# Performance work log

Hardware: AMD Instinct MI355X
Metric: run time of the kernel (lower is better)

Reference implementation:

```python
import jax, jax.numpy as jnp
import numpy as np

D_MODEL = 512
D_AUX = 64
B, N = 8, 2048


def setup_inputs() -> dict:
    key = jax.random.key(0)
    ks = jax.random.split(key, 12)
    lim = 1.0 / np.sqrt(D_MODEL)  # torch Linear default init scale
    inp = {
        "x": jax.random.normal(ks[0], (B, N, D_MODEL), dtype=jnp.float32),
        "query_aux": jax.random.normal(ks[1], (B, N, D_AUX), dtype=jnp.float32),
        "key_aux": jax.random.normal(ks[2], (B, N, D_AUX), dtype=jnp.float32),
        "adjacency_mask": jax.random.randint(ks[3], (B, N, N), 0, 2, dtype=jnp.int32),
        "merge_coefficients": jnp.float32(0.3),
        "Wq": jax.random.uniform(ks[4], (D_MODEL, D_MODEL), jnp.float32, -lim, lim),
        "bq": jax.random.uniform(ks[5], (D_MODEL,), jnp.float32, -lim, lim),
        "Wk": jax.random.uniform(ks[6], (D_MODEL, D_MODEL), jnp.float32, -lim, lim),
        "bk": jax.random.uniform(ks[7], (D_MODEL,), jnp.float32, -lim, lim),
        "Wv": jax.random.uniform(ks[8], (D_MODEL, D_MODEL), jnp.float32, -lim, lim),
        "bv": jax.random.uniform(ks[9], (D_MODEL,), jnp.float32, -lim, lim),
        "threshold": jnp.float32(0.5),
    }
    return inp


def reference(x, query_aux, key_aux, adjacency_mask, merge_coefficients,
              Wq, bq, Wk, bk, Wv, bv, threshold):
    d_model = x.shape[-1]
    d_aux = key_aux.shape[-1]
    scale = jnp.asarray(d_model, x.dtype) ** 0.5
    scale_aux = jnp.asarray(d_aux, x.dtype) ** 0.5

    q = x @ Wq.T + bq  # [B,N,D]
    k = x @ Wk.T + bk
    v = x @ Wv.T + bv

    scores = jnp.einsum('bnd,bmd->bnm', q, k) / scale  # [B,N,N]
    scores_aux = jnp.einsum('bnd,bmd->bnm', query_aux, key_aux) / scale_aux

    # data-dependent merge: where aux score nonzero AND score above learned threshold
    merge_mask = (scores_aux != 0) & (scores > threshold)
    merged = (1.0 - merge_coefficients) * scores + merge_coefficients * scores_aux
    scores = jnp.where(merge_mask, merged, scores)

    mask_value = jnp.finfo(scores.dtype).min
    scores = jnp.where(adjacency_mask == 0, mask_value, scores)

    weights = jax.nn.softmax(scores, axis=-1)
    return jnp.einsum('bnm,bmd->bnd', weights, v)
```

## Files before the change

kernel.cpp:

```cpp
#include <hip/hip_runtime.h>
#include <cstdint>

#define SEQ    2048
#define DM     512
#define DAUX   64

typedef _Float16 f16;
typedef __attribute__((ext_vector_type(2))) _Float16 f16x2;
typedef __attribute__((ext_vector_type(4))) _Float16 f16x4;
typedef __attribute__((ext_vector_type(8))) _Float16 f16x8;
typedef __attribute__((ext_vector_type(4))) float fx4;
typedef __attribute__((ext_vector_type(16))) float fx16;

__device__ __forceinline__ void g2l16(const void* g, void* l) {
  __builtin_amdgcn_global_load_lds(
      (__attribute__((address_space(1))) void*)const_cast<void*>(g),
      (__attribute__((address_space(3))) void*)l, 16, 0, 0);
}

__device__ __forceinline__ void stagec(const f16* __restrict__ hi,
                                       const f16* __restrict__ lo,
                                       int stride, f16* lds, int t) {
#pragma unroll
  for (int p = 0; p < 4; ++p) {
    int L = p * 256 + t;
    int row = L >> 3, jb = L & 7;
    int jl = jb ^ (row & 7);
    const f16* src = (jl < 4) ? hi + (size_t)row * stride + jl * 8
                              : lo + (size_t)row * stride + (jl - 4) * 8;
    g2l16(src, lds + L * 8);
  }
}
__device__ __forceinline__ f16x8 fragc(const f16* lds, int row, int jl) {
  int jp = jl ^ (row & 7);
  return *(const f16x8*)(lds + row * 64 + jp * 8);
}

__device__ __forceinline__ void stage64(const f16* __restrict__ g0, int stride,
                                        f16* lds, int t) {
#pragma unroll
  for (int p = 0; p < 4; ++p) {
    int L = p * 256 + t;
    int row = L >> 3, jb = L & 7;
    int jl = jb ^ (row & 7);
    g2l16(g0 + (size_t)row * stride + jl * 8, lds + L * 8);
  }
}
__device__ __forceinline__ f16x8 frag64(const f16* lds, int row, int kq) {
  int jp = (kq >> 3) ^ (row & 7);
  return *(const f16x8*)(lds + row * 64 + jp * 8);
}

__device__ __forceinline__ void chunk3c(const f16* A, const f16* B,
                                        fx16 acc[2][2], int wm, int wn, int lane) {
  const int r31 = lane & 31;
  const int half8 = (lane >> 5) * 8;
#pragma unroll
  for (int k0 = 0; k0 < 32; k0 += 16) {
    int kb = (k0 + half8) >> 3;
    f16x8 ah[2], al[2];
#pragma unroll
    for (int it = 0; it < 2; ++it) {
      int row = wm * 64 + it * 32 + r31;
      ah[it] = fragc(A, row, kb);
      al[it] = fragc(A, row, kb + 4);
    }
#pragma unroll
    for (int jt = 0; jt < 2; ++jt) {
      int col = wn * 64 + jt * 32 + r31;
      f16x8 bh = fragc(B, col, kb);
      f16x8 bl = fragc(B, col, kb + 4);
#pragma unroll
      for (int it = 0; it < 2; ++it) {
        acc[it][jt] = __builtin_amdgcn_mfma_f32_32x32x16_f16(ah[it], bh, acc[it][jt], 0, 0, 0);
        acc[it][jt] = __builtin_amdgcn_mfma_f32_32x32x16_f16(ah[it], bl, acc[it][jt], 0, 0, 0);
        acc[it][jt] = __builtin_amdgcn_mfma_f32_32x32x16_f16(al[it], bh, acc[it][jt], 0, 0, 0);
      }
    }
  }
}

__device__ __forceinline__ void chunk1_64(const f16* A, const f16* B,
                                          fx16 acc[2][2], int wm, int wn, int lane) {
  const int r31 = lane & 31;
  const int kq = (lane >> 5) * 8;
#pragma unroll
  for (int k0 = 0; k0 < 64; k0 += 16) {
    f16x8 a[2];
#pragma unroll
    for (int it = 0; it < 2; ++it)
      a[it] = frag64(A, wm * 64 + it * 32 + r31, k0 + kq);
#pragma unroll
    for (int jt = 0; jt < 2; ++jt) {
      f16x8 b = frag64(B, wn * 64 + jt * 32 + r31, k0 + kq);
#pragma unroll
      for (int it = 0; it < 2; ++it)
        acc[it][jt] = __builtin_amdgcn_mfma_f32_32x32x16_f16(a[it], b, acc[it][jt], 0, 0, 0);
    }
  }
}

__global__ __launch_bounds__(256) void convert_split(
    const float* __restrict__ x, const float* __restrict__ Wq,
    const float* __restrict__ Wk, const float* __restrict__ Wv,
    f16* __restrict__ xh, f16* __restrict__ xl,
    f16* __restrict__ Wh, f16* __restrict__ Wl) {
  int idx = blockIdx.x * 256 + threadIdx.x;
  const float* src; f16* dh; f16* dl; size_t off;
  if (idx < 2097152) { src = x; off = (size_t)idx; dh = xh; dl = xl; }
  else {
    int rr = idx - 2097152;
    int w = rr >> 16, o = rr & 65535;
    src = (w == 0) ? Wq : (w == 1) ? Wk : Wv;
    off = (size_t)o;
    dh = Wh + (size_t)w * 262144; dl = Wl + (size_t)w * 262144;
  }
  float4 v = ((const float4*)src)[off];
  float vv[4] = {v.x, v.y, v.z, v.w};
  f16x4 hv, lv;
#pragma unroll
  for (int i = 0; i < 4; ++i) {
    float s = vv[i] * 32.0f;
    f16 hi = (f16)s;
    hv[i] = hi;
    lv[i] = (f16)(s - (float)hi);
  }
  *(f16x4*)(dh + off * 4) = hv;
  *(f16x4*)(dl + off * 4) = lv;
}

__global__ __launch_bounds__(256, 3) void qkv_mfma(
    const f16* __restrict__ xh, const f16* __restrict__ xl,
    const f16* __restrict__ Wh, const f16* __restrict__ Wl,
    const float* __restrict__ bq, const float* __restrict__ bk, const float* __restrict__ bv,
    f16* __restrict__ qh, f16* __restrict__ ql,
    f16* __restrict__ kh, f16* __restrict__ kl,
    f16* __restrict__ vt) {
  __shared__ __align__(16) f16 sm[16384];
  const int t = threadIdx.x;
  const int i0 = blockIdx.x * 128, j0 = blockIdx.y * 128, z = blockIdx.z;
  const f16* WhZ = Wh + (size_t)z * 262144;
  const f16* WlZ = Wl + (size_t)z * 262144;
  const int lane = t & 63, wave = t >> 6;
  const int wm = wave >> 1, wn = wave & 1;
  const int r31 = lane & 31, half = lane >> 5;
  fx16 acc[2][2] = {};
  const f16* xhB = xh + (size_t)i0 * DM;
  const f16* xlB = xl + (size_t)i0 * DM;
  const f16* WhB = WhZ + (size_t)j0 * DM;
  const f16* WlB = WlZ + (size_t)j0 * DM;
  if (z < 2) {
    for (int c = 0; c < 16; ++c) {
      int d0 = c * 32;
      __syncthreads();
      stagec(xhB + d0, xlB + d0, DM, sm, t);
      stagec(WhB + d0, WlB + d0, DM, sm + 8192, t);
      __syncthreads();
      chunk3c(sm, sm + 8192, acc, wm, wn, lane);
    }
  } else {
    for (int c = 0; c < 8; ++c) {
      int d0 = c * 64;
      __syncthreads();
      stage64(xhB + d0, DM, sm, t);
      stage64(WhB + d0, DM, sm + 8192, t);
      __syncthreads();
      chunk1_64(sm, sm + 8192, acc, wm, wn, lane);
    }
  }
  const float* bias = (z == 0) ? bq : (z == 1) ? bk : bv;
  if (z < 2) {
    f16* oh = z ? kh : qh;  f16* ol = z ? kl : ql;
#pragma unroll
    for (int it = 0; it < 2; ++it)
#pragma unroll
      for (int jt = 0; jt < 2; ++jt) {
        int j = j0 + wn * 64 + jt * 32 + r31;
        float bj = bias[j];
#pragma unroll
        for (int r = 0; r < 16; ++r) {
          int ib = i0 + wm * 64 + it * 32 + (r & 3) + 8 * (r >> 2) + 4 * half;
          float val = acc[it][jt][r] * (1.0f / 1024.0f) + bj;
          float s = val * 32.0f;
          f16 hi = (f16)s;
          oh[(size_t)ib * DM + j] = hi;
          ol[(size_t)ib * DM + j] = (f16)(s - (float)hi);
        }
      }
  } else {
#pragma unroll
    for (int it = 0; it < 2; ++it)
#pragma unroll
      for (int jt = 0; jt < 2; ++jt) {
        int j = j0 + wn * 64 + jt * 32 + r31;
        float bj = bias[j];
#pragma unroll
        for (int q4 = 0; q4 < 4; ++q4) {
          int ib = i0 + wm * 64 + it * 32 + 8 * q4 + 4 * half;
          int bb = ib >> 11, nb = ib & 2047;
          f16x4 hv;
#pragma unroll
          for (int g = 0; g < 4; ++g)
            hv[g] = (f16)(acc[it][jt][q4 * 4 + g] * (1.0f / 1024.0f) + bj);
          *(f16x4*)(vt + ((size_t)(bb * DM + j)) * SEQ + nb) = hv;
        }
      }
  }
}

__global__ __launch_bounds__(256, 3) void scores_mfma(
    const f16* __restrict__ qh, const f16* __restrict__ ql,
    const f16* __restrict__ kh, const f16* __restrict__ kl,
    const float* __restrict__ qa, const float* __restrict__ ka,
    const int* __restrict__ adj,
    const float* __restrict__ mc_p, const float* __restrict__ thr_p,
    f16* __restrict__ S16) {
  __shared__ __align__(16) f16 sm[16384];
  const int t = threadIdx.x;
  const int n0 = blockIdx.x * 128, m0 = blockIdx.y * 128, b = blockIdx.z;
  const int lane = t & 63, wave = t >> 6;
  const int wm = wave >> 1, wn = wave & 1;
  const int r31 = lane & 31, half = lane >> 5;
  const int kq = half * 8;

  const f16* qhB = qh + ((size_t)b * SEQ + n0) * DM;
  const f16* qlB = ql + ((size_t)b * SEQ + n0) * DM;
  const f16* khB = kh + ((size_t)b * SEQ + m0) * DM;
  const f16* klB = kl + ((size_t)b * SEQ + m0) * DM;

  fx16 acc[2][2] = {};
  for (int c = 0; c < 16; ++c) {
    int d0 = c * 32;
    __syncthreads();
    stagec(qhB + d0, qlB + d0, DM, sm, t);
    stagec(khB + d0, klB + d0, DM, sm + 8192, t);
    __syncthreads();
    chunk3c(sm, sm + 8192, acc, wm, wn, lane);
  }

  __syncthreads();
  f16* QAl = sm;
  f16* KAl = sm + 8192;
  const float* QAb = qa + ((size_t)b * SEQ + n0) * DAUX;
  const float* KAb = ka + ((size_t)b * SEQ + m0) * DAUX;
#pragma unroll
  for (int p = 0; p < 4; ++p) {
    int L8 = p * 256 + t;
    int row = L8 >> 3, jb = L8 & 7;
    int c8 = jb * 8;
    int jp = jb ^ (row & 7);
    float4 u0 = *(const float4*)(QAb + (size_t)row * DAUX + c8);
    float4 u1 = *(const float4*)(QAb + (size_t)row * DAUX + c8 + 4);
    f16x8 hq = {(f16)u0.x,(f16)u0.y,(f16)u0.z,(f16)u0.w,(f16)u1.x,(f16)u1.y,(f16)u1.z,(f16)u1.w};
    *(f16x8*)(QAl + row * 64 + jp * 8) = hq;
    float4 w0 = *(const float4*)(KAb + (size_t)row * DAUX + c8);
    float4 w1 = *(const float4*)(KAb + (size_t)row * DAUX + c8 + 4);
    f16x8 hk = {(f16)w0.x,(f16)w0.y,(f16)w0.z,(f16)w0.w,(f16)w1.x,(f16)w1.y,(f16)w1.z,(f16)w1.w};
    *(f16x8*)(KAl + row * 64 + jp * 8) = hk;
  }
  __syncthreads();
  fx16 aacc[2][2] = {};
#pragma unroll
  for (int k0 = 0; k0 < 64; k0 += 16) {
    f16x8 qaf[2];
#pragma unroll
    for (int it = 0; it < 2; ++it)
      qaf[it] = frag64(QAl, wm * 64 + it * 32 + r31, k0 + kq);
#pragma unroll
    for (int jt = 0; jt < 2; ++jt) {
      f16x8 kaf = frag64(KAl, wn * 64 + jt * 32 + r31, k0 + kq);
#pragma unroll
      for (int it = 0; it < 2; ++it)
        aacc[it][jt] = __builtin_amdgcn_mfma_f32_32x32x16_f16(qaf[it], kaf, aacc[it][jt], 0, 0, 0);
    }
  }

  const float mc = *mc_p, thr = *thr_p;
  const float invC = 1.0f / (1024.0f * 22.62741699796952f);
#pragma unroll
  for (int it = 0; it < 2; ++it)
#pragma unroll
    for (int jt = 0; jt < 2; ++jt) {
      int col = m0 + wn * 64 + jt * 32 + r31;
#pragma unroll
      for (int r = 0; r < 16; ++r) {
        int row = n0 + wm * 64 + it * 32 + (r & 3) + 8 * (r >> 2) + 4 * half;
        size_t rbase = ((size_t)b * SEQ + row) * SEQ;
        float s = acc[it][jt][r] * invC;
        float sa = aacc[it][jt][r] * 0.125f;
        if (sa != 0.0f && s > thr) s = (1.0f - mc) * s + mc * sa;
        if (adj[rbase + col] == 0) s = -65504.0f;
        S16[rbase + col] = (f16)s;
      }
    }
}

__global__ __launch_bounds__(256) void softmax_p(
    f16* __restrict__ S16, float* __restrict__ rowsum) {
  const int wv = threadIdx.x >> 6, ln = threadIdx.x & 63;
  const size_t row = (size_t)blockIdx.x * 4 + wv;
  f16* Sr = S16 + row * SEQ;
  f16x8 v[4];
  float vals[32];
#pragma unroll
  for (int j = 0; j < 4; ++j) {
    v[j] = *(const f16x8*)(Sr + j * 512 + ln * 8);
#pragma unroll
    for (int i = 0; i < 8; ++i) vals[j * 8 + i] = (float)v[j][i];
  }
  float m = vals[0];
#pragma unroll
  for (int i = 1; i < 32; ++i) m = fmaxf(m, vals[i]);
#pragma unroll
  for (int off = 1; off < 64; off <<= 1) m = fmaxf(m, __shfl_xor(m, off, 64));
  float z = 0.f;
  f16x8 p16[4];
#pragma unroll
  for (int j = 0; j < 4; ++j)
#pragma unroll
    for (int i = 0; i < 8; ++i) {
      f16 p = (f16)(__expf(vals[j * 8 + i] - m) * 1024.0f);
      p16[j][i] = p;
      z += (float)p;
    }
#pragma unroll
  for (int off = 1; off < 64; off <<= 1) z += __shfl_xor(z, off, 64);
  if (ln == 0) rowsum[row] = z;
#pragma unroll
  for (int j = 0; j < 4; ++j)
    *(f16x8*)(Sr + j * 512 + ln * 8) = p16[j];
}

__global__ __launch_bounds__(256, 3) void pv_mfma(
    const f16* __restrict__ P16, const f16* __restrict__ vt,
    const float* __restrict__ rowsum, float* __restrict__ O) {
  __shared__ __align__(16) f16 sm[16384];
  const int t = threadIdx.x;
  const int n0 = blockIdx.x * 128, d0 = blockIdx.y * 128, b = blockIdx.z;
  const int lane = t & 63, wave = t >> 6;
  const int wm = wave >> 1, wn = wave & 1;
  const int r31 = lane & 31, half = lane >> 5;
  fx16 acc[2][2] = {};
  const f16* Pb = P16 + ((size_t)b * SEQ + n0) * SEQ;
  const f16* Vb = vt + ((size_t)b * DM + d0) * SEQ;
  for (int c = 0; c < 32; ++c) {
    int m0 = c * 64;
    __syncthreads();
    stage64(Pb + m0, SEQ, sm, t);
    stage64(Vb + m0, SEQ, sm + 8192, t);
    __syncthreads();
    chunk1_64(sm, sm + 8192, acc, wm, wn, lane);
  }
#pragma unroll
  for (int it = 0; it < 2; ++it)
#pragma unroll
    for (int jt = 0; jt < 2; ++jt) {
      int d = d0 + wn * 64 + jt * 32 + r31;
#pragma unroll
      for (int r = 0; r < 16; ++r) {
        int n = n0 + wm * 64 + it * 32 + (r & 3) + 8 * (r >> 2) + 4 * half;
        float inv = 1.0f / rowsum[(size_t)b * SEQ + n];
        O[((size_t)b * SEQ + n) * DM + d] = acc[it][jt][r] * inv;
      }
    }
}

extern "C" void kernel_launch(void* const* d_in, const int* in_sizes, int n_in,
                              void* d_out, int out_size, void* d_ws, size_t ws_size,
                              hipStream_t stream) {
  const float* x   = (const float*)d_in[0];
  const float* qa  = (const float*)d_in[1];
  const float* ka  = (const float*)d_in[2];
  const int*   adj = (const int*)d_in[3];
  const float* mc  = (const float*)d_in[4];
  const float* Wq  = (const float*)d_in[5];
  const float* bq  = (const float*)d_in[6];
  const float* Wk  = (const float*)d_in[7];
  const float* bk  = (const float*)d_in[8];
  const float* Wv  = (const float*)d_in[9];
  const float* bv  = (const float*)d_in[10];
  const float* thr = (const float*)d_in[11];
  float* out = (float*)d_out;

  f16* qh  = (f16*)d_ws;
  f16* ql  = qh + 8388608;
  f16* kh  = ql + 8388608;
  f16* kl  = kh + 8388608;
  f16* vt  = kl + 8388608;
  f16* S16 = vt + 8388608;
  float* rowsum = (float*)(S16 + 33554432);
  f16* xh = S16;
  f16* xl = xh + 8388608;
  f16* Wh = xl + 8388608;
  f16* Wl = Wh + 786432;

  convert_split<<<8960, 256, 0, stream>>>(x, Wq, Wk, Wv, xh, xl, Wh, Wl);
  qkv_mfma<<<dim3(128, 4, 3), 256, 0, stream>>>(xh, xl, Wh, Wl, bq, bk, bv,
                                                qh, ql, kh, kl, vt);
  scores_mfma<<<dim3(16, 16, 8), 256, 0, stream>>>(qh, ql, kh, kl, qa, ka, adj,
                                                   mc, thr, S16);
  softmax_p<<<4096, 256, 0, stream>>>(S16, rowsum);
  pv_mfma<<<dim3(16, 4, 8), 256, 0, stream>>>(S16, vt, rowsum, out);
}
```

Before: 557.1 us.

## Replace LDS-staged GEMM tiles with register double-buffered direct global loads

```diff
diff --git a/kernel.cpp b/kernel.cpp
--- a/kernel.cpp
+++ b/kernel.cpp
@@ -9,94 +9,69 @@
 typedef __attribute__((ext_vector_type(2))) _Float16 f16x2;
 typedef __attribute__((ext_vector_type(4))) _Float16 f16x4;
 typedef __attribute__((ext_vector_type(8))) _Float16 f16x8;
-typedef __attribute__((ext_vector_type(4))) float fx4;
 typedef __attribute__((ext_vector_type(16))) float fx16;
 
-__device__ __forceinline__ void g2l16(const void* g, void* l) {
-  __builtin_amdgcn_global_load_lds(
-      (__attribute__((address_space(1))) void*)const_cast<void*>(g),
-      (__attribute__((address_space(3))) void*)l, 16, 0, 0);
-}
-
-__device__ __forceinline__ void stagec(const f16* __restrict__ hi,
-                                       const f16* __restrict__ lo,
-                                       int stride, f16* lds, int t) {
-#pragma unroll
-  for (int p = 0; p < 4; ++p) {
-    int L = p * 256 + t;
-    int row = L >> 3, jb = L & 7;
-    int jl = jb ^ (row & 7);
-    const f16* src = (jl < 4) ? hi + (size_t)row * stride + jl * 8
-                              : lo + (size_t)row * stride + (jl - 4) * 8;
-    g2l16(src, lds + L * 8);
-  }
-}
-__device__ __forceinline__ f16x8 fragc(const f16* lds, int row, int jl) {
-  int jp = jl ^ (row & 7);
-  return *(const f16x8*)(lds + row * 64 + jp * 8);
-}
-
-__device__ __forceinline__ void stage64(const f16* __restrict__ g0, int stride,
-                                        f16* lds, int t) {
-#pragma unroll
-  for (int p = 0; p < 4; ++p) {
-    int L = p * 256 + t;
-    int row = L >> 3, jb = L & 7;
-    int jl = jb ^ (row & 7);
-    g2l16(g0 + (size_t)row * stride + jl * 8, lds + L * 8);
-  }
-}
-__device__ __forceinline__ f16x8 frag64(const f16* lds, int row, int kq) {
-  int jp = (kq >> 3) ^ (row & 7);
-  return *(const f16x8*)(lds + row * 64 + jp * 8);
-}
-
-__device__ __forceinline__ void chunk3c(const f16* A, const f16* B,
-                                        fx16 acc[2][2], int wm, int wn, int lane) {
-  const int r31 = lane & 31;
-  const int half8 = (lane >> 5) * 8;
-#pragma unroll
-  for (int k0 = 0; k0 < 32; k0 += 16) {
-    int kb = (k0 + half8) >> 3;
-    f16x8 ah[2], al[2];
-#pragma unroll
-    for (int it = 0; it < 2; ++it) {
-      int row = wm * 64 + it * 32 + r31;
-      ah[it] = fragc(A, row, kb);
-      al[it] = fragc(A, row, kb + 4);
-    }
-#pragma unroll
-    for (int jt = 0; jt < 2; ++jt) {
-      int col = wn * 64 + jt * 32 + r31;
-      f16x8 bh = fragc(B, col, kb);
-      f16x8 bl = fragc(B, col, kb + 4);
-#pragma unroll
-      for (int it = 0; it < 2; ++it) {
-        acc[it][jt] = __builtin_amdgcn_mfma_f32_32x32x16_f16(ah[it], bh, acc[it][jt], 0, 0, 0);
-        acc[it][jt] = __builtin_amdgcn_mfma_f32_32x32x16_f16(ah[it], bl, acc[it][jt], 0, 0, 0);
-        acc[it][jt] = __builtin_amdgcn_mfma_f32_32x32x16_f16(al[it], bh, acc[it][jt], 0, 0, 0);
-      }
-    }
-  }
-}
-
-__device__ __forceinline__ void chunk1_64(const f16* A, const f16* B,
-                                          fx16 acc[2][2], int wm, int wn, int lane) {
-  const int r31 = lane & 31;
-  const int kq = (lane >> 5) * 8;
-#pragma unroll
-  for (int k0 = 0; k0 < 64; k0 += 16) {
-    f16x8 a[2];
-#pragma unroll
-    for (int it = 0; it < 2; ++it)
-      a[it] = frag64(A, wm * 64 + it * 32 + r31, k0 + kq);
-#pragma unroll
-    for (int jt = 0; jt < 2; ++jt) {
-      f16x8 b = frag64(B, wn * 64 + jt * 32 + r31, k0 + kq);
-#pragma unroll
-      for (int it = 0; it < 2; ++it)
-        acc[it][jt] = __builtin_amdgcn_mfma_f32_32x32x16_f16(a[it], b, acc[it][jt], 0, 0, 0);
-    }
+#define MFMA32(a, b, c) __builtin_amdgcn_mfma_f32_32x32x16_f16(a, b, c, 0, 0, 0)
+
+__device__ __forceinline__ void gemm3_regs(
+    const f16* __restrict__ Ah, const f16* __restrict__ Al,
+    const f16* __restrict__ Bh, const f16* __restrict__ Bl,
+    fx16 acc[2][2]) {
+  f16x8 fah[2][2][2], fal[2][2][2], fbh[2][2][2], fbl[2][2][2];
+  auto load3 = [&](int buf, int kb) {
+#pragma unroll
+    for (int i2 = 0; i2 < 2; ++i2)
+#pragma unroll
+      for (int k2 = 0; k2 < 2; ++k2) {
+        fah[buf][i2][k2] = *(const f16x8*)(Ah + (size_t)i2 * 32 * DM + kb + k2 * 16);
+        fal[buf][i2][k2] = *(const f16x8*)(Al + (size_t)i2 * 32 * DM + kb + k2 * 16);
+        fbh[buf][i2][k2] = *(const f16x8*)(Bh + (size_t)i2 * 32 * DM + kb + k2 * 16);
+        fbl[buf][i2][k2] = *(const f16x8*)(Bl + (size_t)i2 * 32 * DM + kb + k2 * 16);
+      }
+  };
+  load3(0, 0);
+#pragma unroll 2
+  for (int c = 0; c < 16; ++c) {
+    int cur = c & 1, nxt = cur ^ 1;
+    load3(nxt, (c + 1) * 32);
+#pragma unroll
+    for (int k = 0; k < 2; ++k)
+#pragma unroll
+      for (int jt = 0; jt < 2; ++jt)
+#pragma unroll
+        for (int it = 0; it < 2; ++it) {
+          acc[it][jt] = MFMA32(fah[cur][it][k], fbh[cur][jt][k], acc[it][jt]);
+          acc[it][jt] = MFMA32(fah[cur][it][k], fbl[cur][jt][k], acc[it][jt]);
+          acc[it][jt] = MFMA32(fal[cur][it][k], fbh[cur][jt][k], acc[it][jt]);
+        }
+  }
+}
+
+template <int NCH, int SA, int SB>
+__device__ __forceinline__ void gemm1_regs(
+    const f16* __restrict__ A, const f16* __restrict__ B, fx16 acc[2][2]) {
+  f16x8 fa[2][2][4], fb[2][2][4];
+  auto load1 = [&](int buf, int kb) {
+#pragma unroll
+    for (int i2 = 0; i2 < 2; ++i2)
+#pragma unroll
+      for (int k2 = 0; k2 < 4; ++k2) {
+        fa[buf][i2][k2] = *(const f16x8*)(A + (size_t)i2 * 32 * SA + kb + k2 * 16);
+        fb[buf][i2][k2] = *(const f16x8*)(B + (size_t)i2 * 32 * SB + kb + k2 * 16);
+      }
+  };
+  load1(0, 0);
+#pragma unroll 2
+  for (int c = 0; c < NCH; ++c) {
+    int cur = c & 1, nxt = cur ^ 1;
+    load1(nxt, (c + 1) * 64);
+#pragma unroll
+    for (int k = 0; k < 4; ++k)
+#pragma unroll
+      for (int jt = 0; jt < 2; ++jt)
+#pragma unroll
+        for (int it = 0; it < 2; ++it)
+          acc[it][jt] = MFMA32(fa[cur][it][k], fb[cur][jt][k], acc[it][jt]);
   }
 }
 
@@ -129,14 +104,13 @@
   *(f16x4*)(dl + off * 4) = lv;
 }
 
-__global__ __launch_bounds__(256, 3) void qkv_mfma(
+__global__ __launch_bounds__(256, 2) void qkv_mfma(
     const f16* __restrict__ xh, const f16* __restrict__ xl,
     const f16* __restrict__ Wh, const f16* __restrict__ Wl,
     const float* __restrict__ bq, const float* __restrict__ bk, const float* __restrict__ bv,
     f16* __restrict__ qh, f16* __restrict__ ql,
     f16* __restrict__ kh, f16* __restrict__ kl,
     f16* __restrict__ vt) {
-  __shared__ __align__(16) f16 sm[16384];
   const int t = threadIdx.x;
   const int i0 = blockIdx.x * 128, j0 = blockIdx.y * 128, z = blockIdx.z;
   const f16* WhZ = Wh + (size_t)z * 262144;
@@ -144,29 +118,15 @@
   const int lane = t & 63, wave = t >> 6;
   const int wm = wave >> 1, wn = wave & 1;
   const int r31 = lane & 31, half = lane >> 5;
+  const int half8 = half * 8;
   fx16 acc[2][2] = {};
-  const f16* xhB = xh + (size_t)i0 * DM;
-  const f16* xlB = xl + (size_t)i0 * DM;
-  const f16* WhB = WhZ + (size_t)j0 * DM;
-  const f16* WlB = WlZ + (size_t)j0 * DM;
+  const size_t arow = (size_t)(i0 + wm * 64 + r31);
+  const size_t brow = (size_t)(j0 + wn * 64 + r31);
   if (z < 2) {
-    for (int c = 0; c < 16; ++c) {
-      int d0 = c * 32;
-      __syncthreads();
-      stagec(xhB + d0, xlB + d0, DM, sm, t);
-      stagec(WhB + d0, WlB + d0, DM, sm + 8192, t);
-      __syncthreads();
-      chunk3c(sm, sm + 8192, acc, wm, wn, lane);
-    }
+    gemm3_regs(xh + arow * DM + half8, xl + arow * DM + half8,
+               WhZ + brow * DM + half8, WlZ + brow * DM + half8, acc);
   } else {
-    for (int c = 0; c < 8; ++c) {
-      int d0 = c * 64;
-      __syncthreads();
-      stage64(xhB + d0, DM, sm, t);
-      stage64(WhB + d0, DM, sm + 8192, t);
-      __syncthreads();
-      chunk1_64(sm, sm + 8192, acc, wm, wn, lane);
-    }
+    gemm1_regs<8, DM, DM>(xh + arow * DM + half8, WhZ + brow * DM + half8, acc);
   }
   const float* bias = (z == 0) ? bq : (z == 1) ? bk : bv;
   if (z < 2) {
@@ -208,72 +168,59 @@
   }
 }
 
-__global__ __launch_bounds__(256, 3) void scores_mfma(
+__global__ __launch_bounds__(256, 2) void scores_mfma(
     const f16* __restrict__ qh, const f16* __restrict__ ql,
     const f16* __restrict__ kh, const f16* __restrict__ kl,
     const float* __restrict__ qa, const float* __restrict__ ka,
     const int* __restrict__ adj,
     const float* __restrict__ mc_p, const float* __restrict__ thr_p,
     f16* __restrict__ S16) {
-  __shared__ __align__(16) f16 sm[16384];
   const int t = threadIdx.x;
   const int n0 = blockIdx.x * 128, m0 = blockIdx.y * 128, b = blockIdx.z;
   const int lane = t & 63, wave = t >> 6;
   const int wm = wave >> 1, wn = wave & 1;
   const int r31 = lane & 31, half = lane >> 5;
-  const int kq = half * 8;
-
-  const f16* qhB = qh + ((size_t)b * SEQ + n0) * DM;
-  const f16* qlB = ql + ((size_t)b * SEQ + n0) * DM;
-  const f16* khB = kh + ((size_t)b * SEQ + m0) * DM;
-  const f16* klB = kl + ((size_t)b * SEQ + m0) * DM;
+  const int half8 = half * 8;
+
+  f16x2 sax2[2][2][8];
+  {
+    fx16 aacc[2][2] = {};
+    const float* QAp = qa + ((size_t)b * SEQ + n0 + wm * 64 + r31) * DAUX + half8;
+    const float* KAp = ka + ((size_t)b * SEQ + m0 + wn * 64 + r31) * DAUX + half8;
+#pragma unroll
+    for (int k0 = 0; k0 < 64; k0 += 16) {
+      f16x8 qaf[2], kaf[2];
+#pragma unroll
+      for (int i2 = 0; i2 < 2; ++i2) {
+        const float* p = QAp + (size_t)i2 * 32 * DAUX + k0;
+        float4 u0 = *(const float4*)p, u1 = *(const float4*)(p + 4);
+        qaf[i2] = f16x8{(f16)u0.x, (f16)u0.y, (f16)u0.z, (f16)u0.w,
+                        (f16)u1.x, (f16)u1.y, (f16)u1.z, (f16)u1.w};
+        const float* p2 = KAp + (size_t)i2 * 32 * DAUX + k0;
+        float4 w0 = *(const float4*)p2, w1 = *(const float4*)(p2 + 4);
+        kaf[i2] = f16x8{(f16)w0.x, (f16)w0.y, (f16)w0.z, (f16)w0.w,
+                        (f16)w1.x, (f16)w1.y, (f16)w1.z, (f16)w1.w};
+      }
+#pragma unroll
+      for (int jt = 0; jt < 2; ++jt)
+#pragma unroll
+        for (int it = 0; it < 2; ++it)
+          aacc[it][jt] = MFMA32(qaf[it], kaf[jt], aacc[it][jt]);
+    }
+#pragma unroll
+    for (int it = 0; it < 2; ++it)
+#pragma unroll
+      for (int jt = 0; jt < 2; ++jt)
+#pragma unroll
+        for (int r = 0; r < 16; ++r)
+          sax2[it][jt][r >> 1][r & 1] = (f16)aacc[it][jt][r];
+  }
 
   fx16 acc[2][2] = {};
-  for (int c = 0; c < 16; ++c) {
-    int d0 = c * 32;
-    __syncthreads();
-    stagec(qhB + d0, qlB + d0, DM, sm, t);
-    stagec(khB + d0, klB + d0, DM, sm + 8192, t);
-    __syncthreads();
-    chunk3c(sm, sm + 8192, acc, wm, wn, lane);
-  }
-
-  __syncthreads();
-  f16* QAl = sm;
-  f16* KAl = sm + 8192;
-  const float* QAb = qa + ((size_t)b * SEQ + n0) * DAUX;
-  const float* KAb = ka + ((size_t)b * SEQ + m0) * DAUX;
-#pragma unroll
-  for (int p = 0; p < 4; ++p) {
-    int L8 = p * 256 + t;
-    int row = L8 >> 3, jb = L8 & 7;
-    int c8 = jb * 8;
-    int jp = jb ^ (row & 7);
-    float4 u0 = *(const float4*)(QAb + (size_t)row * DAUX + c8);
-    float4 u1 = *(const float4*)(QAb + (size_t)row * DAUX + c8 + 4);
-    f16x8 hq = {(f16)u0.x,(f16)u0.y,(f16)u0.z,(f16)u0.w,(f16)u1.x,(f16)u1.y,(f16)u1.z,(f16)u1.w};
-    *(f16x8*)(QAl + row * 64 + jp * 8) = hq;
-    float4 w0 = *(const float4*)(KAb + (size_t)row * DAUX + c8);
-    float4 w1 = *(const float4*)(KAb + (size_t)row * DAUX + c8 + 4);
-    f16x8 hk = {(f16)w0.x,(f16)w0.y,(f16)w0.z,(f16)w0.w,(f16)w1.x,(f16)w1.y,(f16)w1.z,(f16)w1.w};
-    *(f16x8*)(KAl + row * 64 + jp * 8) = hk;
-  }
-  __syncthreads();
-  fx16 aacc[2][2] = {};
-#pragma unroll
-  for (int k0 = 0; k0 < 64; k0 += 16) {
-    f16x8 qaf[2];
-#pragma unroll
-    for (int it = 0; it < 2; ++it)
-      qaf[it] = frag64(QAl, wm * 64 + it * 32 + r31, k0 + kq);
-#pragma unroll
-    for (int jt = 0; jt < 2; ++jt) {
-      f16x8 kaf = frag64(KAl, wn * 64 + jt * 32 + r31, k0 + kq);
-#pragma unroll
-      for (int it = 0; it < 2; ++it)
-        aacc[it][jt] = __builtin_amdgcn_mfma_f32_32x32x16_f16(qaf[it], kaf, aacc[it][jt], 0, 0, 0);
-    }
-  }
+  const size_t arow = (size_t)b * SEQ + n0 + wm * 64 + r31;
+  const size_t brow = (size_t)b * SEQ + m0 + wn * 64 + r31;
+  gemm3_regs(qh + arow * DM + half8, ql + arow * DM + half8,
+             kh + brow * DM + half8, kl + brow * DM + half8, acc);
 
   const float mc = *mc_p, thr = *thr_p;
   const float invC = 1.0f / (1024.0f * 22.62741699796952f);
@@ -287,7 +234,7 @@
         int row = n0 + wm * 64 + it * 32 + (r & 3) + 8 * (r >> 2) + 4 * half;
         size_t rbase = ((size_t)b * SEQ + row) * SEQ;
         float s = acc[it][jt][r] * invC;
-        float sa = aacc[it][jt][r] * 0.125f;
+        float sa = (float)sax2[it][jt][r >> 1][r & 1] * 0.125f;
         if (sa != 0.0f && s > thr) s = (1.0f - mc) * s + mc * sa;
         if (adj[rbase + col] == 0) s = -65504.0f;
         S16[rbase + col] = (f16)s;
@@ -331,26 +278,19 @@
     *(f16x8*)(Sr + j * 512 + ln * 8) = p16[j];
 }
 
-__global__ __launch_bounds__(256, 3) void pv_mfma(
+__global__ __launch_bounds__(256, 2) void pv_mfma(
     const f16* __restrict__ P16, const f16* __restrict__ vt,
     const float* __restrict__ rowsum, float* __restrict__ O) {
-  __shared__ __align__(16) f16 sm[16384];
   const int t = threadIdx.x;
   const int n0 = blockIdx.x * 128, d0 = blockIdx.y * 128, b = blockIdx.z;
   const int lane = t & 63, wave = t >> 6;
   const int wm = wave >> 1, wn = wave & 1;
   const int r31 = lane & 31, half = lane >> 5;
+  const int half8 = half * 8;
   fx16 acc[2][2] = {};
-  const f16* Pb = P16 + ((size_t)b * SEQ + n0) * SEQ;
-  const f16* Vb = vt + ((size_t)b * DM + d0) * SEQ;
-  for (int c = 0; c < 32; ++c) {
-    int m0 = c * 64;
-    __syncthreads();
-    stage64(Pb + m0, SEQ, sm, t);
-    stage64(Vb + m0, SEQ, sm + 8192, t);
-    __syncthreads();
-    chunk1_64(sm, sm + 8192, acc, wm, wn, lane);
-  }
+  const f16* Ap = P16 + ((size_t)b * SEQ + n0 + wm * 64 + r31) * SEQ + half8;
+  const f16* Bp = vt + ((size_t)b * DM + d0 + wn * 64 + r31) * SEQ + half8;
+  gemm1_regs<32, SEQ, SEQ>(Ap, Bp, acc);
 #pragma unroll
   for (int it = 0; it < 2; ++it)
 #pragma unroll
```

New measurement: 842.8 us. 51.3% more time.
